# Kernel optimization log

Measured on AMD Instinct MI355X. Metric: run time of the kernel, lower is better.

## Reference

```python
import jax, jax.numpy as jnp
import numpy as np
import math

B, S, H = 4, 2048, 1024
EMBED_DIM = 1024


def setup_inputs() -> dict:
    key = jax.random.key(0)
    ks = jax.random.split(key, 7)
    scale = 1.0 / math.sqrt(H)
    return {
        "xs": jax.random.normal(ks[0], (B, S, H), dtype=jnp.float32),
        "WQ_w": jax.random.normal(ks[1], (EMBED_DIM, H), dtype=jnp.float32) * scale,
        "WQ_b": jax.random.normal(ks[2], (EMBED_DIM,), dtype=jnp.float32) * scale,
        "WK_w": jax.random.normal(ks[3], (EMBED_DIM, H), dtype=jnp.float32) * scale,
        "WK_b": jax.random.normal(ks[4], (EMBED_DIM,), dtype=jnp.float32) * scale,
        "WV_w": jax.random.normal(ks[5], (EMBED_DIM, H), dtype=jnp.float32) * scale,
        "WV_b": jax.random.normal(ks[6], (EMBED_DIM,), dtype=jnp.float32) * scale,
    }


def reference(xs, WQ_w, WQ_b, WK_w, WK_b, WV_w, WV_b):
    # Linear projections (torch nn.Linear: x @ W.T + b)
    q = jnp.einsum('bsh,eh->bse', xs, WQ_w) + WQ_b  # [B,S,E]
    k = jnp.einsum('bsh,eh->bse', xs, WK_w) + WK_b
    v = jnp.einsum('bsh,eh->bse', xs, WV_w) + WV_b
    seq_len = xs.shape[1]
    inv_sqrt_e = 1.0 / math.sqrt(EMBED_DIM)
    qk = jnp.einsum('bqe,bke->bqk', q, k) * inv_sqrt_e  # [B,S,S]
    # causal mask: positions k > q get -inf (triu, diagonal=1)
    causal = jnp.tril(jnp.ones((seq_len, seq_len), dtype=bool))
    qk = jnp.where(causal[None, :, :], qk, -jnp.inf)
    attn = jax.nn.softmax(qk, axis=2)
    y = jnp.einsum('bqk,bke->bqe', attn, v)  # [B,S,E]
    return y
```

## Files before the change

kernel.cpp:

```cpp
#include <hip/hip_runtime.h>
#include <cstdint>
#include <cstddef>

typedef _Float16 f16;
typedef __attribute__((ext_vector_type(4))) _Float16 f16x4;
typedef __attribute__((ext_vector_type(8))) _Float16 f16x8;
typedef __attribute__((ext_vector_type(4))) float f32x4;

static constexpr int BB = 4;
static constexpr int SS = 2048;
static constexpr int EE = 1024;

static constexpr int BM = 128, BN = 128;

__device__ __forceinline__ void gload_lds16(const f16* g, f16* l) {
  __builtin_amdgcn_global_load_lds(
      (const __attribute__((address_space(1))) void*)g,
      (__attribute__((address_space(3))) void*)l, 16, 0, 0);
}

struct Frag {
  int lane, wave, wy, wx, l16, quad, quadx;
  __device__ Frag() {
    const int tid = threadIdx.x;
    lane = tid & 63; wave = tid >> 6;
    wy = wave >> 1; wx = wave & 1;
    l16 = lane & 15; quad = lane >> 4;
    quadx = quad ^ ((l16 >> 2) & 3);
  }
};

struct Stager {
  const f16* g[2];
  int l[2];
  __device__ void init(const f16* base, int ld, const Frag& fr) {
#pragma unroll
    for (int i = 0; i < 2; ++i) {
      const int c = fr.wave * 128 + i * 64 + fr.lane;
      const int row = c >> 2;
      const int kcs = (c & 3) ^ ((c >> 4) & 3);
      g[i] = base + (size_t)row * ld + kcs * 8;
      l[i] = c * 8;
    }
  }
  __device__ __forceinline__ void stage(int ko, f16* lds) const {
    gload_lds16(g[0] + ko, lds + l[0]);
    gload_lds16(g[1] + ko, lds + l[1]);
  }
};

__device__ __forceinline__ void mfma_round(
    const f16* __restrict__ Ash, const f16* __restrict__ Bsh,
    f32x4 acc[4][4], const Frag& fr)
{
  f16x8 af[4], bf[4];
#pragma unroll
  for (int mi = 0; mi < 4; ++mi)
    af[mi] = *(const f16x8*)(Ash + (fr.wy * 64 + mi * 16 + fr.l16) * 32 + fr.quadx * 8);
#pragma unroll
  for (int ni = 0; ni < 4; ++ni)
    bf[ni] = *(const f16x8*)(Bsh + (fr.wx * 64 + ni * 16 + fr.l16) * 32 + fr.quadx * 8);
#pragma unroll
  for (int mi = 0; mi < 4; ++mi)
#pragma unroll
    for (int ni = 0; ni < 4; ++ni)
      acc[mi][ni] = __builtin_amdgcn_mfma_f32_16x16x32_f16(af[mi], bf[ni], acc[mi][ni], 0, 0, 0);
}

__device__ __forceinline__ void gemm_core_k(
    const f16* __restrict__ A, const f16* __restrict__ Bt,
    int lda, int ldb, int kstart, int kcount,
    f16* __restrict__ Ash, f16* __restrict__ Bsh,
    f32x4 acc[4][4], const Frag& fr)
{
  Stager sa, sb;
  sa.init(A, lda, fr);
  sb.init(Bt, ldb, fr);
  for (int kt = 0; kt < kcount; ++kt) {
    const int ko = (kstart + kt) * 64;
    sa.stage(ko, Ash);       sa.stage(ko + 32, Ash + 128 * 32);
    sb.stage(ko, Bsh);       sb.stage(ko + 32, Bsh + 128 * 32);
    __syncthreads();
    mfma_round(Ash, Bsh, acc, fr);
    mfma_round(Ash + 128 * 32, Bsh + 128 * 32, acc, fr);
    __syncthreads();
  }
}

__device__ __forceinline__ void gemm_core(
    const f16* __restrict__ A, const f16* __restrict__ Bt,
    int lda, int ldb, int kOuter,
    f16* __restrict__ Ash, f16* __restrict__ Bsh,
    f32x4 acc[4][4], const Frag& fr)
{
  gemm_core_k(A, Bt, lda, ldb, 0, kOuter, Ash, Bsh, acc, fr);
}

__global__ __launch_bounds__(256) void cast_all_kernel(
    const float* __restrict__ xs,
    const float* __restrict__ w0, const float* __restrict__ w1, const float* __restrict__ w2,
    f16* __restrict__ Xh, f16* __restrict__ o0, f16* __restrict__ o1, f16* __restrict__ o2,
    float* __restrict__ Y)
{
  const int i = blockIdx.x * 256 + threadIdx.x;
  if (i >= 2883584) {
    const float4 z = {0.f, 0.f, 0.f, 0.f};
    ((float4*)Y)[i - 2883584] = z;
    return;
  }
  const float* src; f16* dst; int idx;
  if (i < 2097152) {
    src = xs; dst = Xh; idx = i;
  } else {
    const int j = i - 2097152;
    const int w = j >> 18;
    idx = j & 262143;
    src = (w == 0) ? w0 : (w == 1) ? w1 : w2;
    dst = (w == 0) ? o0 : (w == 1) ? o1 : o2;
  }
  const float4 f = ((const float4*)src)[idx];
  f16x4 h;
  h.x = (f16)f.x; h.y = (f16)f.y; h.z = (f16)f.z; h.w = (f16)f.w;
  ((f16x4*)dst)[idx] = h;
}

__global__ __launch_bounds__(256, 2) void proj_kernel(
    const f16* __restrict__ X,
    const f16* __restrict__ Wq, const f16* __restrict__ Wk, const f16* __restrict__ Wv,
    const float* __restrict__ bq, const float* __restrict__ bk, const float* __restrict__ bv,
    f16* __restrict__ Qh, f16* __restrict__ Kh, f16* __restrict__ Vt)
{
  __shared__ __align__(16) f16 smem[3][2][BM * 32];
  Frag fr;
  const int t = blockIdx.x;
  if (t < 512) {
    const int row0 = (t & 63) * BM, col0 = (t >> 6) * BN;
    Stager sa, sw0, sw1;
    sa.init(X + (size_t)row0 * EE, EE, fr);
    sw0.init(Wq + (size_t)col0 * EE, EE, fr);
    sw1.init(Wk + (size_t)col0 * EE, EE, fr);

    f32x4 acc[2][4][4] = {};

    for (int kt = 0; kt < EE / 64; ++kt) {
      const int ko = kt * 64;
      sa.stage(ko, smem[0][0]);   sa.stage(ko + 32, smem[0][1]);
      sw0.stage(ko, smem[1][0]);  sw0.stage(ko + 32, smem[1][1]);
      sw1.stage(ko, smem[2][0]);  sw1.stage(ko + 32, smem[2][1]);
      __syncthreads();
#pragma unroll
      for (int h = 0; h < 2; ++h) {
        f16x8 af[4];
#pragma unroll
        for (int mi = 0; mi < 4; ++mi)
          af[mi] = *(const f16x8*)(smem[0][h] + (fr.wy * 64 + mi * 16 + fr.l16) * 32 + fr.quadx * 8);
#pragma unroll
        for (int z = 0; z < 2; ++z) {
          f16x8 bf[4];
#pragma unroll
          for (int ni = 0; ni < 4; ++ni)
            bf[ni] = *(const f16x8*)(smem[1 + z][h] + (fr.wx * 64 + ni * 16 + fr.l16) * 32 + fr.quadx * 8);
#pragma unroll
          for (int mi = 0; mi < 4; ++mi)
#pragma unroll
            for (int ni = 0; ni < 4; ++ni)
              acc[z][mi][ni] = __builtin_amdgcn_mfma_f32_16x16x32_f16(af[mi], bf[ni], acc[z][mi][ni], 0, 0, 0);
        }
      }
      __syncthreads();
    }

#pragma unroll
    for (int z = 0; z < 2; ++z) {
      const float* bias = (z == 0) ? bq : bk;
      f16* out = (z == 0) ? Qh : Kh;
#pragma unroll
      for (int ni = 0; ni < 4; ++ni) {
        const int c = col0 + fr.wx * 64 + ni * 16 + fr.l16;
        const float bv2 = bias[c];
#pragma unroll
        for (int mi = 0; mi < 4; ++mi) {
          const int r = row0 + fr.wy * 64 + mi * 16 + fr.quad * 4;
#pragma unroll
          for (int i = 0; i < 4; ++i)
            out[(size_t)(r + i) * EE + c] = (f16)(acc[z][mi][ni][i] + bv2);
        }
      }
    }
  } else {
    const int u = t - 512;
    const int row0 = (u & 7) * BM;
    const int sg0 = (u >> 3) * BN;
    const int b = sg0 / SS, s0 = sg0 % SS;
    f32x4 acc[4][4] = {};
    gemm_core(Wv + (size_t)row0 * EE, X + (size_t)sg0 * EE, EE, EE, EE / 64,
              smem[0][0], smem[1][0], acc, fr);
    f16* out = Vt + (size_t)b * EE * SS;
#pragma unroll
    for (int ni = 0; ni < 4; ++ni) {
      const int c = s0 + fr.wx * 64 + ni * 16 + fr.l16;
#pragma unroll
      for (int mi = 0; mi < 4; ++mi) {
        const int r = row0 + fr.wy * 64 + mi * 16 + fr.quad * 4;
#pragma unroll
        for (int i = 0; i < 4; ++i)
          out[(size_t)(r + i) * SS + c] = (f16)(acc[mi][ni][i] + bv[r + i]);
      }
    }
  }
}

__global__ __launch_bounds__(256) void scores_kernel(
    const f16* __restrict__ Q, const f16* __restrict__ Kh, f16* __restrict__ Sc)
{
  __shared__ __align__(16) f16 Ash[2][BM * 32];
  __shared__ __align__(16) f16 Bsh[2][BN * 32];
  const int t = blockIdx.x, b = blockIdx.z;
  int qt = 0;
  while ((qt + 1) * (qt + 2) / 2 <= t) ++qt;
  const int kt = t - qt * (qt + 1) / 2;
  const f16* A  = Q  + (size_t)b * SS * EE + (size_t)qt * BM * EE;
  const f16* Bp = Kh + (size_t)b * SS * EE + (size_t)kt * BN * EE;
  f16* out = Sc + (size_t)b * SS * SS;
  Frag fr;
  f32x4 acc[4][4] = {};
  gemm_core(A, Bp, EE, EE, EE / 64, Ash[0], Bsh[0], acc, fr);
  const float scale = 0.03125f;
#pragma unroll
  for (int ni = 0; ni < 4; ++ni) {
    const int c = kt * BN + fr.wx * 64 + ni * 16 + fr.l16;
#pragma unroll
    for (int mi = 0; mi < 4; ++mi) {
      const int r = qt * BM + fr.wy * 64 + mi * 16 + fr.quad * 4;
#pragma unroll
      for (int i = 0; i < 4; ++i)
        out[(size_t)(r + i) * SS + c] = (f16)(acc[mi][ni][i] * scale);
    }
  }
}

__global__ __launch_bounds__(256) void softmax_kernel(f16* __restrict__ Sc)
{
  const int q = blockIdx.x, b = blockIdx.y;
  f16* row = Sc + (size_t)b * SS * SS + (size_t)q * SS;
  const int n = q + 1;
  const int kend = ((q >> 7) + 1) << 7;
  const int tid = threadIdx.x;
  const int i0 = tid * 8;

  float v[8];
  if (i0 + 8 <= n) {
    const f16x8 h = *(const f16x8*)(row + i0);
#pragma unroll
    for (int j = 0; j < 8; ++j) v[j] = (float)h[j];
  } else {
#pragma unroll
    for (int j = 0; j < 8; ++j) {
      const int idx = i0 + j;
      v[j] = (idx < n) ? (float)row[idx] : -1e30f;
    }
  }

  float m = v[0];
#pragma unroll
  for (int j = 1; j < 8; ++j) m = fmaxf(m, v[j]);
  __shared__ float red[4];
#pragma unroll
  for (int off = 32; off > 0; off >>= 1) m = fmaxf(m, __shfl_down(m, off));
  if ((tid & 63) == 0) red[tid >> 6] = m;
  __syncthreads();
  m = fmaxf(fmaxf(red[0], red[1]), fmaxf(red[2], red[3]));

  float sum = 0.f;
#pragma unroll
  for (int j = 0; j < 8; ++j) {
    v[j] = (i0 + j < n) ? __expf(v[j] - m) : 0.f;
    sum += v[j];
  }
#pragma unroll
  for (int off = 32; off > 0; off >>= 1) sum += __shfl_down(sum, off);
  __syncthreads();
  if ((tid & 63) == 0) red[tid >> 6] = sum;
  __syncthreads();
  sum = red[0] + red[1] + red[2] + red[3];
  const float inv = 1.f / sum;

  if (i0 < kend) {
    f16x8 h;
#pragma unroll
    for (int j = 0; j < 8; ++j) h[j] = (f16)(v[j] * inv);
    *(f16x8*)(row + i0) = h;
  }
}

__global__ __launch_bounds__(256) void pv_kernel(
    const f16* __restrict__ P, const f16* __restrict__ Vt, float* __restrict__ Y)
{
  __shared__ __align__(16) f16 Ash[2][BM * 32];
  __shared__ __align__(16) f16 Bsh[2][BN * 32];
  const int t = blockIdx.x;
  const int u = t & 255;
  const int qh = u & 7, et = (u >> 3) & 7, b = u >> 6;
  const int seg = t >> 8;
  const int qhi = 15 - qh;
  const int Uhi = (qhi + 1) * 2;
  const int Ulo = (qh + 1) * 2;
  const f16* Pb = P + (size_t)b * SS * SS;
  const f16* Bp = Vt + (size_t)b * EE * SS + (size_t)et * BN * SS;
  float* out = Y + (size_t)b * SS * EE;
  Frag fr;

  if (seg == 0) {
    f32x4 acc[4][4] = {};
    gemm_core_k(Pb + (size_t)qhi * BM * SS, Bp, SS, SS, 0, 17, Ash[0], Bsh[0], acc, fr);
#pragma unroll
    for (int ni = 0; ni < 4; ++ni) {
      const int c = et * BN + fr.wx * 64 + ni * 16 + fr.l16;
#pragma unroll
      for (int mi = 0; mi < 4; ++mi) {
        const int r = qhi * BM + fr.wy * 64 + mi * 16 + fr.quad * 4;
#pragma unroll
        for (int i = 0; i < 4; ++i)
          atomicAdd(&out[(size_t)(r + i) * EE + c], acc[mi][ni][i]);
      }
    }
  } else {
    {
      f32x4 acc[4][4] = {};
      gemm_core_k(Pb + (size_t)qhi * BM * SS, Bp, SS, SS, 17, Uhi - 17, Ash[0], Bsh[0], acc, fr);
#pragma unroll
      for (int ni = 0; ni < 4; ++ni) {
        const int c = et * BN + fr.wx * 64 + ni * 16 + fr.l16;
#pragma unroll
        for (int mi = 0; mi < 4; ++mi) {
          const int r = qhi * BM + fr.wy * 64 + mi * 16 + fr.quad * 4;
#pragma unroll
          for (int i = 0; i < 4; ++i)
            atomicAdd(&out[(size_t)(r + i) * EE + c], acc[mi][ni][i]);
        }
      }
    }
    {
      f32x4 acc[4][4] = {};
      gemm_core_k(Pb + (size_t)qh * BM * SS, Bp, SS, SS, 0, Ulo, Ash[0], Bsh[0], acc, fr);
#pragma unroll
      for (int ni = 0; ni < 4; ++ni) {
        const int c = et * BN + fr.wx * 64 + ni * 16 + fr.l16;
#pragma unroll
        for (int mi = 0; mi < 4; ++mi) {
          const int r = qh * BM + fr.wy * 64 + mi * 16 + fr.quad * 4;
#pragma unroll
          for (int i = 0; i < 4; ++i)
            out[(size_t)(r + i) * EE + c] = acc[mi][ni][i];
        }
      }
    }
  }
}

extern "C" void kernel_launch(void* const* d_in, const int* in_sizes, int n_in,
                              void* d_out, int out_size, void* d_ws, size_t ws_size,
                              hipStream_t stream)
{
  const float* xs  = (const float*)d_in[0];
  const float* WQw = (const float*)d_in[1];
  const float* WQb = (const float*)d_in[2];
  const float* WKw = (const float*)d_in[3];
  const float* WKb = (const float*)d_in[4];
  const float* WVw = (const float*)d_in[5];
  const float* WVb = (const float*)d_in[6];

  const size_t ME = (size_t)BB * SS * EE;
  const size_t WE = (size_t)EE * EE;

  f16* Xh = (f16*)d_ws;
  f16* Wq = Xh + ME;
  f16* Wk = Wq + WE;
  f16* Wv = Wk + WE;
  f16* Qh = Wv + WE;
  f16* Kh = Qh + ME;
  f16* Vt = Kh + ME;
  f16* Sc = Vt + ME;

  cast_all_kernel<<<dim3(19456), 256, 0, stream>>>(
      xs, WQw, WKw, WVw, Xh, Wq, Wk, Wv, (float*)d_out);

  proj_kernel<<<dim3(1024), 256, 0, stream>>>(
      Xh, Wq, Wk, Wv, WQb, WKb, WVb, Qh, Kh, Vt);

  const int nTri = (SS / BM) * (SS / BM + 1) / 2;
  scores_kernel<<<dim3(nTri, 1, BB), 256, 0, stream>>>(Qh, Kh, Sc);

  softmax_kernel<<<dim3(SS, BB), 256, 0, stream>>>(Sc);

  pv_kernel<<<dim3(512), 256, 0, stream>>>(Sc, Vt, (float*)d_out);
}
```

Measured before the change: 265.4 us.

## Fuse scores, softmax and PV into one persistent kernel with grid barriers

Replaces the three separate scores, softmax and PV launches with one 512-block persistent kernel that uses atomic-counter grid barriers between phases. Softmax now runs one row per wavefront using shuffle reductions, with no block-level shared-memory reduction. The aim is to remove launch gaps and tail imbalance between stages. The grid barrier only works if all 512 blocks are co-resident, which is not guaranteed and would deadlock otherwise. Block 0..31 also do an extra score tile, so the first phase is uneven.

Result: slower. 438.6 us (+65.3%).

```diff
diff --git a/kernel.cpp b/kernel.cpp
--- a/kernel.cpp
+++ b/kernel.cpp
@@ -96,13 +96,25 @@
   gemm_core_k(A, Bt, lda, ldb, 0, kOuter, Ash, Bsh, acc, fr);
 }
 
+__device__ __forceinline__ void grid_bar(int* cnt, int nblk) {
+  __syncthreads();
+  if (threadIdx.x == 0) {
+    __threadfence();
+    atomicAdd(cnt, 1);
+    while (atomicAdd(cnt, 0) < nblk) __builtin_amdgcn_s_sleep(2);
+  }
+  __syncthreads();
+  __threadfence();
+}
+
 __global__ __launch_bounds__(256) void cast_all_kernel(
     const float* __restrict__ xs,
     const float* __restrict__ w0, const float* __restrict__ w1, const float* __restrict__ w2,
     f16* __restrict__ Xh, f16* __restrict__ o0, f16* __restrict__ o1, f16* __restrict__ o2,
-    float* __restrict__ Y)
+    float* __restrict__ Y, int* __restrict__ bar)
 {
   const int i = blockIdx.x * 256 + threadIdx.x;
+  if (i < 2) bar[i] = 0;
   if (i >= 2883584) {
     const float4 z = {0.f, 0.f, 0.f, 0.f};
     ((float4*)Y)[i - 2883584] = z;
@@ -210,21 +222,19 @@
   }
 }
 
-__global__ __launch_bounds__(256) void scores_kernel(
-    const f16* __restrict__ Q, const f16* __restrict__ Kh, f16* __restrict__ Sc)
-{
-  __shared__ __align__(16) f16 Ash[2][BM * 32];
-  __shared__ __align__(16) f16 Bsh[2][BN * 32];
-  const int t = blockIdx.x, b = blockIdx.z;
+__device__ __forceinline__ void score_tile(
+    const f16* __restrict__ Q, const f16* __restrict__ Kh, f16* __restrict__ Sc,
+    int item, f16* Ash, f16* Bsh, const Frag& fr)
+{
+  const int b = item / 136, tt = item - b * 136;
   int qt = 0;
-  while ((qt + 1) * (qt + 2) / 2 <= t) ++qt;
-  const int kt = t - qt * (qt + 1) / 2;
+  while ((qt + 1) * (qt + 2) / 2 <= tt) ++qt;
+  const int kt = tt - qt * (qt + 1) / 2;
   const f16* A  = Q  + (size_t)b * SS * EE + (size_t)qt * BM * EE;
   const f16* Bp = Kh + (size_t)b * SS * EE + (size_t)kt * BN * EE;
   f16* out = Sc + (size_t)b * SS * SS;
-  Frag fr;
   f32x4 acc[4][4] = {};
-  gemm_core(A, Bp, EE, EE, EE / 64, Ash[0], Bsh[0], acc, fr);
+  gemm_core(A, Bp, EE, EE, EE / 64, Ash, Bsh, acc, fr);
   const float scale = 0.03125f;
 #pragma unroll
   for (int ni = 0; ni < 4; ++ni) {
@@ -239,95 +249,84 @@
   }
 }
 
-__global__ __launch_bounds__(256) void softmax_kernel(f16* __restrict__ Sc)
-{
-  const int q = blockIdx.x, b = blockIdx.y;
-  f16* row = Sc + (size_t)b * SS * SS + (size_t)q * SS;
-  const int n = q + 1;
-  const int kend = ((q >> 7) + 1) << 7;
-  const int tid = threadIdx.x;
-  const int i0 = tid * 8;
-
-  float v[8];
-  if (i0 + 8 <= n) {
-    const f16x8 h = *(const f16x8*)(row + i0);
-#pragma unroll
-    for (int j = 0; j < 8; ++j) v[j] = (float)h[j];
-  } else {
-#pragma unroll
-    for (int j = 0; j < 8; ++j) {
-      const int idx = i0 + j;
-      v[j] = (idx < n) ? (float)row[idx] : -1e30f;
-    }
-  }
-
-  float m = v[0];
-#pragma unroll
-  for (int j = 1; j < 8; ++j) m = fmaxf(m, v[j]);
-  __shared__ float red[4];
-#pragma unroll
-  for (int off = 32; off > 0; off >>= 1) m = fmaxf(m, __shfl_down(m, off));
-  if ((tid & 63) == 0) red[tid >> 6] = m;
-  __syncthreads();
-  m = fmaxf(fmaxf(red[0], red[1]), fmaxf(red[2], red[3]));
-
-  float sum = 0.f;
-#pragma unroll
-  for (int j = 0; j < 8; ++j) {
-    v[j] = (i0 + j < n) ? __expf(v[j] - m) : 0.f;
-    sum += v[j];
-  }
-#pragma unroll
-  for (int off = 32; off > 0; off >>= 1) sum += __shfl_down(sum, off);
-  __syncthreads();
-  if ((tid & 63) == 0) red[tid >> 6] = sum;
-  __syncthreads();
-  sum = red[0] + red[1] + red[2] + red[3];
-  const float inv = 1.f / sum;
-
-  if (i0 < kend) {
-    f16x8 h;
-#pragma unroll
-    for (int j = 0; j < 8; ++j) h[j] = (f16)(v[j] * inv);
-    *(f16x8*)(row + i0) = h;
-  }
-}
-
-__global__ __launch_bounds__(256) void pv_kernel(
-    const f16* __restrict__ P, const f16* __restrict__ Vt, float* __restrict__ Y)
+__global__ __launch_bounds__(256) void attn_kernel(
+    const f16* __restrict__ Q, const f16* __restrict__ Kh, f16* __restrict__ Sc,
+    const f16* __restrict__ Vt, float* __restrict__ Y, int* __restrict__ bar)
 {
   __shared__ __align__(16) f16 Ash[2][BM * 32];
   __shared__ __align__(16) f16 Bsh[2][BN * 32];
+  Frag fr;
   const int t = blockIdx.x;
-  const int u = t & 255;
-  const int qh = u & 7, et = (u >> 3) & 7, b = u >> 6;
-  const int seg = t >> 8;
-  const int qhi = 15 - qh;
-  const int Uhi = (qhi + 1) * 2;
-  const int Ulo = (qh + 1) * 2;
-  const f16* Pb = P + (size_t)b * SS * SS;
-  const f16* Bp = Vt + (size_t)b * EE * SS + (size_t)et * BN * SS;
-  float* out = Y + (size_t)b * SS * EE;
-  Frag fr;
-
-  if (seg == 0) {
-    f32x4 acc[4][4] = {};
-    gemm_core_k(Pb + (size_t)qhi * BM * SS, Bp, SS, SS, 0, 17, Ash[0], Bsh[0], acc, fr);
-#pragma unroll
-    for (int ni = 0; ni < 4; ++ni) {
-      const int c = et * BN + fr.wx * 64 + ni * 16 + fr.l16;
-#pragma unroll
-      for (int mi = 0; mi < 4; ++mi) {
-        const int r = qhi * BM + fr.wy * 64 + mi * 16 + fr.quad * 4;
-#pragma unroll
-        for (int i = 0; i < 4; ++i)
-          atomicAdd(&out[(size_t)(r + i) * EE + c], acc[mi][ni][i]);
-      }
-    }
-  } else {
-    {
+
+  score_tile(Q, Kh, Sc, t, Ash[0], Bsh[0], fr);
+  if (t < 32) score_tile(Q, Kh, Sc, 512 + t, Ash[0], Bsh[0], fr);
+
+  grid_bar(&bar[0], 512);
+
+  {
+    const int gw = t * 4 + fr.wave;
+#pragma unroll
+    for (int j = 0; j < 4; ++j) {
+      const int r = gw * 4 + j;
+      const int b = r >> 11, q = r & 2047;
+      f16* row = Sc + (size_t)b * SS * SS + (size_t)q * SS;
+      const int n = q + 1;
+      const int kend = ((q >> 7) + 1) << 7;
+      float v[4][8];
+      float m = -1e30f;
+#pragma unroll
+      for (int c = 0; c < 4; ++c) {
+        const int base = c * 512 + fr.lane * 8;
+        const f16x8 h = *(const f16x8*)(row + base);
+#pragma unroll
+        for (int e = 0; e < 8; ++e) {
+          v[c][e] = (base + e < n) ? (float)h[e] : -1e30f;
+          m = fmaxf(m, v[c][e]);
+        }
+      }
+#pragma unroll
+      for (int off = 32; off > 0; off >>= 1) m = fmaxf(m, __shfl_xor(m, off));
+      float s = 0.f;
+#pragma unroll
+      for (int c = 0; c < 4; ++c)
+#pragma unroll
+        for (int e = 0; e < 8; ++e) {
+          const int base = c * 512 + fr.lane * 8;
+          v[c][e] = (base + e < n) ? __expf(v[c][e] - m) : 0.f;
+          s += v[c][e];
+        }
+#pragma unroll
+      for (int off = 32; off > 0; off >>= 1) s += __shfl_xor(s, off);
+      const float inv = 1.f / s;
+#pragma unroll
+      for (int c = 0; c < 4; ++c) {
+        const int base = c * 512 + fr.lane * 8;
+        if (base < kend) {
+          f16x8 h;
+#pragma unroll
+          for (int e = 0; e < 8; ++e) h[e] = (f16)(v[c][e] * inv);
+          *(f16x8*)(row + base) = h;
+        }
+      }
+    }
+  }
+
+  grid_bar(&bar[1], 512);
+
+  {
+    const int u = t & 255;
+    const int qh = u & 7, et = (u >> 3) & 7, b = u >> 6;
+    const int seg = t >> 8;
+    const int qhi = 15 - qh;
+    const int Uhi = (qhi + 1) * 2;
+    const int Ulo = (qh + 1) * 2;
+    const f16* Pb = Sc + (size_t)b * SS * SS;
+    const f16* Bp = Vt + (size_t)b * EE * SS + (size_t)et * BN * SS;
+    float* out = Y + (size_t)b * SS * EE;
+
+    if (seg == 0) {
       f32x4 acc[4][4] = {};
-      gemm_core_k(Pb + (size_t)qhi * BM * SS, Bp, SS, SS, 17, Uhi - 17, Ash[0], Bsh[0], acc, fr);
+      gemm_core_k(Pb + (size_t)qhi * BM * SS, Bp, SS, SS, 0, 17, Ash[0], Bsh[0], acc, fr);
 #pragma unroll
       for (int ni = 0; ni < 4; ++ni) {
         const int c = et * BN + fr.wx * 64 + ni * 16 + fr.l16;
@@ -339,19 +338,35 @@
             atomicAdd(&out[(size_t)(r + i) * EE + c], acc[mi][ni][i]);
         }
       }
-    }
-    {
-      f32x4 acc[4][4] = {};
-      gemm_core_k(Pb + (size_t)qh * BM * SS, Bp, SS, SS, 0, Ulo, Ash[0], Bsh[0], acc, fr);
-#pragma unroll
-      for (int ni = 0; ni < 4; ++ni) {
-        const int c = et * BN + fr.wx * 64 + ni * 16 + fr.l16;
-#pragma unroll
-        for (int mi = 0; mi < 4; ++mi) {
-          const int r = qh * BM + fr.wy * 64 + mi * 16 + fr.quad * 4;
-#pragma unroll
-          for (int i = 0; i < 4; ++i)
-            out[(size_t)(r + i) * EE + c] = acc[mi][ni][i];
+    } else {
+      {
+        f32x4 acc[4][4] = {};
+        gemm_core_k(Pb + (size_t)qhi * BM * SS, Bp, SS, SS, 17, Uhi - 17, Ash[0], Bsh[0], acc, fr);
+#pragma unroll
+        for (int ni = 0; ni < 4; ++ni) {
+          const int c = et * BN + fr.wx * 64 + ni * 16 + fr.l16;
+#pragma unroll
+          for (int mi = 0; mi < 4; ++mi) {
+            const int r = qhi * BM + fr.wy * 64 + mi * 16 + fr.quad * 4;
+#pragma unroll
+            for (int i = 0; i < 4; ++i)
+              atomicAdd(&out[(size_t)(r + i) * EE + c], acc[mi][ni][i]);
+          }
+        }
+      }
+      {
+        f32x4 acc[4][4] = {};
+        gemm_core_k(Pb + (size_t)qh * BM * SS, Bp, SS, SS, 0, Ulo, Ash[0], Bsh[0], acc, fr);
+#pragma unroll
+        for (int ni = 0; ni < 4; ++ni) {
+          const int c = et * BN + fr.wx * 64 + ni * 16 + fr.l16;
+#pragma unroll
+          for (int mi = 0; mi < 4; ++mi) {
+            const int r = qh * BM + fr.wy * 64 + mi * 16 + fr.quad * 4;
+#pragma unroll
+            for (int i = 0; i < 4; ++i)
+              out[(size_t)(r + i) * EE + c] = acc[mi][ni][i];
+          }
         }
       }
     }
@@ -381,17 +396,14 @@
   f16* Kh = Qh + ME;
   f16* Vt = Kh + ME;
   f16* Sc = Vt + ME;
+  int* bar = (int*)(Sc + (size_t)BB * SS * SS);
 
   cast_all_kernel<<<dim3(19456), 256, 0, stream>>>(
-      xs, WQw, WKw, WVw, Xh, Wq, Wk, Wv, (float*)d_out);
+      xs, WQw, WKw, WVw, Xh, Wq, Wk, Wv, (float*)d_out, bar);
 
   proj_kernel<<<dim3(1024), 256, 0, stream>>>(
       Xh, Wq, Wk, Wv, WQb, WKb, WVb, Qh, Kh, Vt);
 
-  const int nTri = (SS / BM) * (SS / BM + 1) / 2;
-  scores_kernel<<<dim3(nTri, 1, BB), 256, 0, stream>>>(Qh, Kh, Sc);
-
-  softmax_kernel<<<dim3(SS, BB), 256, 0, stream>>>(Sc);
-
-  pv_kernel<<<dim3(512), 256, 0, stream>>>(Sc, Vt, (float*)d_out);
-}
+  attn_kernel<<<dim3(512), 256, 0, stream>>>(
+      Qh, Kh, Sc, Vt, (float*)d_out, bar);
+}
```
